# Kernel optimization log

Hardware: AMD Instinct MI355X
Metric: run time of the kernel (lower is better)

The kernel has to match this reference:

```python
import jax, jax.numpy as jnp
import numpy as np

N_NODES = 100000
N_EDGES = 1600000
IN_FEATS = 64
OUT_FEATS = 100


def setup_inputs() -> dict:
    key = jax.random.key(0)
    k1, k2, k3, k4 = jax.random.split(key, 4)
    e = jax.random.normal(k1, (N_EDGES, IN_FEATS), dtype=jnp.float32)
    dst = jax.random.randint(k2, (N_EDGES,), 0, N_NODES, dtype=jnp.int32)
    W = jax.random.normal(k3, (OUT_FEATS, IN_FEATS), dtype=jnp.float32) * (1.0 / np.sqrt(IN_FEATS))
    b = jax.random.normal(k4, (OUT_FEATS,), dtype=jnp.float32) * 0.01
    return {"e": e, "dst": dst, "W": W, "b": b, "n_nodes": N_NODES}


def reference(e, dst, W, b, n_nodes):
    # edge linear projection: f = e @ W^T + b  -> [n_edges, out_feats]
    f = jnp.einsum("ei,oi->eo", e, W) + b
    # copy_e + mean reduce: segment-mean of edge features into dst nodes
    sums = jax.ops.segment_sum(f, dst, num_segments=n_nodes)  # [n_nodes, out]
    deg = jax.ops.segment_sum(jnp.ones((f.shape[0],), dtype=f.dtype), dst,
                              num_segments=n_nodes)  # in-degree per node
    # DGL mean reducer yields 0 for zero-in-degree nodes
    h = sums / jnp.maximum(deg, 1.0)[:, None]
    return h
```

## Files before the change

### kernel.cpp

```cpp
#include <hip/hip_runtime.h>

#define N_NODES 100000
#define N_EDGES 1600000
#define IN_F    64
#define OUT_F   100

#define K_BUCKETS 1563
#define NBLK      500
#define EPB       3200
#define SCAN_LEN  (K_BUCKETS * NBLK)
#define SCH       2048
#define SB        ((SCAN_LEN + SCH - 1) / SCH)
#define CAP       3072

#define OFF_CNT   0
#define OFF_PART  (SCAN_LEN * 4)
#define OFF_BIN   (SCAN_LEN * 4 + 2048)
#define WS_NEEDED (OFF_BIN + N_EDGES * 4)

#define FB_DEG     0
#define FB_OFFS    524288
#define FB_CURSOR  1048576
#define FB_GCUR    1572864
#define FB_EIDS    1573888

__global__ void __launch_bounds__(256) k_count(const int* __restrict__ dst,
                                               int* __restrict__ cnt) {
    __shared__ int h[K_BUCKETS];
    for (int i = threadIdx.x; i < K_BUCKETS; i += 256) h[i] = 0;
    __syncthreads();
    int base = blockIdx.x * EPB;
    #pragma unroll
    for (int it = 0; it < 3; it++) {
        int i = base + it * 1024 + threadIdx.x * 4;
        int4 d = *(const int4*)(dst + i);
        atomicAdd(&h[d.x >> 6], 1);
        atomicAdd(&h[d.y >> 6], 1);
        atomicAdd(&h[d.z >> 6], 1);
        atomicAdd(&h[d.w >> 6], 1);
    }
    if (threadIdx.x < 128) {
        int i = base + 3072 + threadIdx.x;
        atomicAdd(&h[dst[i] >> 6], 1);
    }
    __syncthreads();
    for (int k = threadIdx.x; k < K_BUCKETS; k += 256)
        cnt[k * NBLK + blockIdx.x] = h[k];
}

__global__ void k_s1(const int* __restrict__ cnt, int* __restrict__ part) {
    __shared__ int ws_[4];
    int b0 = blockIdx.x * SCH;
    int t = threadIdx.x;
    int tot = 0;
    #pragma unroll
    for (int i = 0; i < 8; i++) {
        int idx = b0 + i * 256 + t;
        if (idx < SCAN_LEN) tot += cnt[idx];
    }
    #pragma unroll
    for (int off = 32; off; off >>= 1) tot += __shfl_down(tot, off, 64);
    if ((t & 63) == 0) ws_[t >> 6] = tot;
    __syncthreads();
    if (t == 0) part[blockIdx.x] = ws_[0] + ws_[1] + ws_[2] + ws_[3];
}

__global__ void k_s2(int* __restrict__ part) {
    int lane = threadIdx.x;
    int carry = 0;
    for (int b0 = 0; b0 < SB; b0 += 64) {
        int idx = b0 + lane;
        int v = (idx < SB) ? part[idx] : 0;
        int x = v;
        #pragma unroll
        for (int off = 1; off < 64; off <<= 1) {
            int y = __shfl_up(x, off, 64);
            if (lane >= off) x += y;
        }
        int tot = __shfl(x, 63, 64);
        if (idx < SB) part[idx] = carry + x - v;
        carry += tot;
    }
}

__global__ void k_s3(int* __restrict__ cnt, const int* __restrict__ part) {
    __shared__ int wsum[4];
    int t = threadIdx.x, lane = t & 63, w = t >> 6;
    int idx0 = blockIdx.x * SCH + t * 8;
    int v[8];
    int s = 0;
    #pragma unroll
    for (int i = 0; i < 8; i++) {
        v[i] = (idx0 + i < SCAN_LEN) ? cnt[idx0 + i] : 0;
        s += v[i];
    }
    int x = s;
    #pragma unroll
    for (int off = 1; off < 64; off <<= 1) {
        int y = __shfl_up(x, off, 64);
        if (lane >= off) x += y;
    }
    if (lane == 63) wsum[w] = x;
    __syncthreads();
    int wb = 0;
    for (int i = 0; i < w; i++) wb += wsum[i];
    int run = part[blockIdx.x] + wb + (x - s);
    #pragma unroll
    for (int i = 0; i < 8; i++) {
        int tmp = v[i];
        if (idx0 + i < SCAN_LEN) cnt[idx0 + i] = run;
        run += tmp;
    }
}

__global__ void __launch_bounds__(256) k_bin(const int* __restrict__ dst,
                                             const int* __restrict__ scn,
                                             int* __restrict__ binned) {
    __shared__ int cur[K_BUCKETS];
    for (int k = threadIdx.x; k < K_BUCKETS; k += 256)
        cur[k] = scn[k * NBLK + blockIdx.x];
    __syncthreads();
    int base = blockIdx.x * EPB;
    #pragma unroll
    for (int it = 0; it < 3; it++) {
        int i = base + it * 1024 + threadIdx.x * 4;
        int4 d = *(const int4*)(dst + i);
        int p;
        p = atomicAdd(&cur[d.x >> 6], 1); binned[p] = ((d.x & 63) << 21) | i;
        p = atomicAdd(&cur[d.y >> 6], 1); binned[p] = ((d.y & 63) << 21) | (i + 1);
        p = atomicAdd(&cur[d.z >> 6], 1); binned[p] = ((d.z & 63) << 21) | (i + 2);
        p = atomicAdd(&cur[d.w >> 6], 1); binned[p] = ((d.w & 63) << 21) | (i + 3);
    }
    if (threadIdx.x < 128) {
        int i = base + 3072 + threadIdx.x;
        int d = dst[i];
        int p = atomicAdd(&cur[d >> 6], 1);
        binned[p] = ((d & 63) << 21) | i;
    }
}

__global__ void __launch_bounds__(256, 2) k_fused(
        const float* __restrict__ e, const int* __restrict__ binned,
        const int* __restrict__ scn, const float* __restrict__ W,
        const float* __restrict__ b, float* __restrict__ out) {
    __shared__ int   deg[64];
    __shared__ int   lofs[64];
    __shared__ int   sorted[CAP];
    __shared__ __align__(16) float srow[4][64];

    int tid = threadIdx.x, lane = tid & 63, w = tid >> 6;
    int sub = lane & 15, g = lane >> 4;
    int bk = blockIdx.x;
    int base = scn[bk * NBLK];
    int end  = (bk + 1 < K_BUCKETS) ? scn[(bk + 1) * NBLK] : N_EDGES;
    int cntb = end - base;

    for (int i = tid; i < 64; i += 256) deg[i] = 0;
    __syncthreads();

    bool fast = (cntb <= CAP);
    if (fast) {
        int pk[12], rk[12];
        int nI = (cntb + 255) >> 8;
        for (int i = 0; i < nI; i++) {
            int idx = tid + i * 256;
            if (idx < cntb) {
                int p = binned[base + idx];
                pk[i] = p;
                rk[i] = atomicAdd(&deg[p >> 21], 1);
            } else pk[i] = -1;
        }
        __syncthreads();
        if (w == 0) {
            int d = deg[lane];
            int x = d;
            #pragma unroll
            for (int off = 1; off < 64; off <<= 1) {
                int y = __shfl_up(x, off, 64);
                if (lane >= off) x += y;
            }
            lofs[lane] = x - d;
        }
        __syncthreads();
        for (int i = 0; i < nI; i++) {
            if (pk[i] >= 0) {
                int lid = pk[i] >> 21;
                sorted[lofs[lid] + rk[i]] = pk[i] & 0x1FFFFF;
            }
        }
        __syncthreads();
    }

    int row1 = 64 + lane;
    if (row1 >= OUT_F) row1 = 0;
    float w0[IN_F], w1[IN_F];
    const float4* W4 = (const float4*)W;
    #pragma unroll
    for (int j = 0; j < IN_F / 4; j++) {
        float4 t0 = W4[lane * (IN_F / 4) + j];
        w0[4*j+0] = t0.x; w0[4*j+1] = t0.y; w0[4*j+2] = t0.z; w0[4*j+3] = t0.w;
        float4 t1 = W4[row1 * (IN_F / 4) + j];
        w1[4*j+0] = t1.x; w1[4*j+1] = t1.y; w1[4*j+2] = t1.z; w1[4*j+3] = t1.w;
    }
    float bb0 = b[lane];
    float bb1 = b[row1];

    const float4* e4 = (const float4*)e;

    for (int t = 0; t < 16; t++) {
        int lid = w * 16 + t;
        int node = bk * 64 + lid;
        if (node >= N_NODES) break;

        int c;
        float* sr = &srow[w][0];

        if (fast) {
            int o = lofs[lid];
            c = deg[lid];
            if (c > 0) {
                float4 a0 = {0,0,0,0}, a1 = {0,0,0,0}, a2 = {0,0,0,0}, a3 = {0,0,0,0};
                for (int cb = 0; cb < c; cb += 64) {
                    int cc = c - cb; if (cc > 64) cc = 64;
                    int ng = (cc + 3) >> 2;
                    int ob = o + cb;
                    for (int i = 0; i < ng; i += 4) {
                        int idx0 = (i + 0) * 4 + g;
                        int idx1 = (i + 1) * 4 + g;
                        int idx2 = (i + 2) * 4 + g;
                        int idx3 = (i + 3) * 4 + g;
                        int c1 = cc - 1;
                        int e0 = sorted[ob + ((idx0 < c1) ? idx0 : c1)];
                        int e1 = sorted[ob + ((idx1 < c1) ? idx1 : c1)];
                        int e2 = sorted[ob + ((idx2 < c1) ? idx2 : c1)];
                        int e3 = sorted[ob + ((idx3 < c1) ? idx3 : c1)];
                        float4 v0 = e4[(size_t)e0 * 16 + sub];
                        float4 v1 = e4[(size_t)e1 * 16 + sub];
                        float4 v2 = e4[(size_t)e2 * 16 + sub];
                        float4 v3 = e4[(size_t)e3 * 16 + sub];
                        float m0 = (idx0 < cc) ? 1.0f : 0.0f;
                        float m1 = (idx1 < cc) ? 1.0f : 0.0f;
                        float m2 = (idx2 < cc) ? 1.0f : 0.0f;
                        float m3 = (idx3 < cc) ? 1.0f : 0.0f;
                        a0.x = fmaf(v0.x, m0, a0.x); a0.y = fmaf(v0.y, m0, a0.y);
                        a0.z = fmaf(v0.z, m0, a0.z); a0.w = fmaf(v0.w, m0, a0.w);
                        a1.x = fmaf(v1.x, m1, a1.x); a1.y = fmaf(v1.y, m1, a1.y);
                        a1.z = fmaf(v1.z, m1, a1.z); a1.w = fmaf(v1.w, m1, a1.w);
                        a2.x = fmaf(v2.x, m2, a2.x); a2.y = fmaf(v2.y, m2, a2.y);
                        a2.z = fmaf(v2.z, m2, a2.z); a2.w = fmaf(v2.w, m2, a2.w);
                        a3.x = fmaf(v3.x, m3, a3.x); a3.y = fmaf(v3.y, m3, a3.y);
                        a3.z = fmaf(v3.z, m3, a3.z); a3.w = fmaf(v3.w, m3, a3.w);
                    }
                }
                float4 s;
                s.x = (a0.x + a1.x) + (a2.x + a3.x);
                s.y = (a0.y + a1.y) + (a2.y + a3.y);
                s.z = (a0.z + a1.z) + (a2.z + a3.z);
                s.w = (a0.w + a1.w) + (a2.w + a3.w);
                s.x += __shfl_xor(s.x, 16, 64);
                s.y += __shfl_xor(s.y, 16, 64);
                s.z += __shfl_xor(s.z, 16, 64);
                s.w += __shfl_xor(s.w, 16, 64);
                s.x += __shfl_xor(s.x, 32, 64);
                s.y += __shfl_xor(s.y, 32, 64);
                s.z += __shfl_xor(s.z, 32, 64);
                s.w += __shfl_xor(s.w, 32, 64);
                float inv = 1.0f / (float)c;
                s.x *= inv; s.y *= inv; s.z *= inv; s.w *= inv;
                if (g == 0) ((float4*)sr)[sub] = s;
            }
        } else {
            c = 0;
            float s0 = 0.f;
            for (int j0 = 0; j0 < cntb; j0 += 64) {
                int idx = j0 + lane;
                int p = (idx < cntb) ? binned[base + idx] : -1;
                bool m = (p >= 0) && ((p >> 21) == lid);
                unsigned long long msk = __ballot(m);
                c += __popcll(msk);
                while (msk) {
                    int l = __ffsll((long long)msk) - 1;
                    msk &= msk - 1;
                    int eid = __builtin_amdgcn_readlane(p, l) & 0x1FFFFF;
                    s0 += e[((size_t)eid << 6) + lane];
                }
            }
            if (c > 0) sr[lane] = s0 * (1.0f / (float)c);
        }

        float h0 = 0.0f, h1 = 0.0f;
        if (c > 0) {
            float aa0 = 0.f, aa1 = 0.f;
            const float4* sr4 = (const float4*)sr;
            #pragma unroll
            for (int q = 0; q < 16; q++) {
                float4 f = sr4[q];
                aa0 = fmaf(f.x, w0[4*q+0], aa0);  aa1 = fmaf(f.x, w1[4*q+0], aa1);
                aa0 = fmaf(f.y, w0[4*q+1], aa0);  aa1 = fmaf(f.y, w1[4*q+1], aa1);
                aa0 = fmaf(f.z, w0[4*q+2], aa0);  aa1 = fmaf(f.z, w1[4*q+2], aa1);
                aa0 = fmaf(f.w, w0[4*q+3], aa0);  aa1 = fmaf(f.w, w1[4*q+3], aa1);
            }
            h0 = aa0 + bb0;
            h1 = aa1 + bb1;
        }

        size_t ob2 = (size_t)node * OUT_F;
        out[ob2 + lane] = h0;
        if (lane < OUT_F - 64) out[ob2 + 64 + lane] = h1;
    }
}

__global__ void fb_hist(const int* __restrict__ dst, int* __restrict__ deg) {
    int i = (blockIdx.x * blockDim.x + threadIdx.x) * 4;
    if (i + 3 < N_EDGES) {
        int4 d = *(const int4*)(dst + i);
        atomicAdd(&deg[d.x], 1); atomicAdd(&deg[d.y], 1);
        atomicAdd(&deg[d.z], 1); atomicAdd(&deg[d.w], 1);
    } else {
        for (int k = i; k < N_EDGES; k++) atomicAdd(&deg[dst[k]], 1);
    }
}

__global__ void fb_scan(const int* __restrict__ deg, int* __restrict__ offs,
                        int* __restrict__ cursor, int* __restrict__ gcur) {
    int n = blockIdx.x * blockDim.x + threadIdx.x;
    int lane = threadIdx.x & 63;
    int d = (n < N_NODES) ? deg[n] : 0;
    int x = d;
    #pragma unroll
    for (int off = 1; off < 64; off <<= 1) {
        int y = __shfl_up(x, off, 64);
        if (lane >= off) x += y;
    }
    int excl = x - d;
    int total = __shfl(x, 63, 64);
    int bs = 0;
    if (lane == 63) bs = atomicAdd(gcur, total);
    bs = __shfl(bs, 63, 64);
    if (n < N_NODES) {
        offs[n] = bs + excl;
        cursor[n] = bs + excl;
    }
}

__global__ void fb_scatter(const int* __restrict__ dst, int* __restrict__ cursor,
                           int* __restrict__ eids) {
    int i = (blockIdx.x * blockDim.x + threadIdx.x) * 4;
    if (i + 3 < N_EDGES) {
        int4 d = *(const int4*)(dst + i);
        int p0 = atomicAdd(&cursor[d.x], 1);
        int p1 = atomicAdd(&cursor[d.y], 1);
        int p2 = atomicAdd(&cursor[d.z], 1);
        int p3 = atomicAdd(&cursor[d.w], 1);
        eids[p0] = i; eids[p1] = i + 1; eids[p2] = i + 2; eids[p3] = i + 3;
    } else {
        for (int k = i; k < N_EDGES; k++) {
            int pos = atomicAdd(&cursor[dst[k]], 1);
            eids[pos] = k;
        }
    }
}

__global__ void __launch_bounds__(256) fb_gather(
        const float* __restrict__ e, const int* __restrict__ eids,
        const int* __restrict__ offs, const int* __restrict__ deg,
        const float* __restrict__ W, const float* __restrict__ b,
        float* __restrict__ out, int n_waves_total) {
    __shared__ float srow[4][64];
    int lane = threadIdx.x & 63, w = (threadIdx.x >> 6) & 3;
    int wid  = (blockIdx.x * blockDim.x + threadIdx.x) >> 6;
    int row1 = 64 + lane;
    if (row1 >= OUT_F) row1 = 0;
    float w0[IN_F], w1[IN_F];
    const float4* W4 = (const float4*)W;
    #pragma unroll
    for (int j = 0; j < IN_F / 4; j++) {
        float4 t0 = W4[lane * (IN_F / 4) + j];
        w0[4*j+0] = t0.x; w0[4*j+1] = t0.y; w0[4*j+2] = t0.z; w0[4*j+3] = t0.w;
        float4 t1 = W4[row1 * (IN_F / 4) + j];
        w1[4*j+0] = t1.x; w1[4*j+1] = t1.y; w1[4*j+2] = t1.z; w1[4*j+3] = t1.w;
    }
    float bb0 = b[lane];
    float bb1 = b[row1];
    for (int n = wid; n < N_NODES; n += n_waves_total) {
        int o = __builtin_amdgcn_readfirstlane(offs[n]);
        int c = __builtin_amdgcn_readfirstlane(deg[n]);
        float s0 = 0.f, s1 = 0.f;
        for (int cb = 0; cb < c; cb += 64) {
            int cc = c - cb; if (cc > 64) cc = 64;
            int myeid = 0;
            if (lane < cc) myeid = eids[o + cb + lane];
            for (int j = 0; j < cc; j += 2) {
                int i0 = __builtin_amdgcn_readlane(myeid, j);
                s0 += e[((size_t)i0 << 6) + lane];
                if (j + 1 < cc) {
                    int i1 = __builtin_amdgcn_readlane(myeid, j + 1);
                    s1 += e[((size_t)i1 << 6) + lane];
                }
            }
        }
        float* sr = &srow[w][0];
        sr[lane] = (s0 + s1) * ((c > 0) ? 1.0f / (float)c : 0.0f);
        float a0 = 0.f, a1 = 0.f;
        const float4* sr4 = (const float4*)sr;
        #pragma unroll
        for (int q = 0; q < 16; q++) {
            float4 f = sr4[q];
            a0 = fmaf(f.x, w0[4*q+0], a0);  a1 = fmaf(f.x, w1[4*q+0], a1);
            a0 = fmaf(f.y, w0[4*q+1], a0);  a1 = fmaf(f.y, w1[4*q+1], a1);
            a0 = fmaf(f.z, w0[4*q+2], a0);  a1 = fmaf(f.z, w1[4*q+2], a1);
            a0 = fmaf(f.w, w0[4*q+3], a0);  a1 = fmaf(f.w, w1[4*q+3], a1);
        }
        float h0 = (c > 0) ? a0 + bb0 : 0.0f;
        float h1 = (c > 0) ? a1 + bb1 : 0.0f;
        size_t ob = (size_t)n * OUT_F;
        out[ob + lane] = h0;
        if (lane < OUT_F - 64) out[ob + 64 + lane] = h1;
    }
}

extern "C" void kernel_launch(void* const* d_in, const int* in_sizes, int n_in,
                              void* d_out, int out_size, void* d_ws, size_t ws_size,
                              hipStream_t stream) {
    const float* e   = (const float*)d_in[0];
    const int*   dst = (const int*)d_in[1];
    const float* W   = (const float*)d_in[2];
    const float* b   = (const float*)d_in[3];
    float* out = (float*)d_out;
    char* ws = (char*)d_ws;

    if (ws_size >= (size_t)WS_NEEDED) {
        int* cnt    = (int*)(ws + OFF_CNT);
        int* part   = (int*)(ws + OFF_PART);
        int* binned = (int*)(ws + OFF_BIN);

        k_count<<<NBLK, 256, 0, stream>>>(dst, cnt);
        k_s1   <<<SB, 256, 0, stream>>>(cnt, part);
        k_s2   <<<1, 64, 0, stream>>>(part);
        k_s3   <<<SB, 256, 0, stream>>>(cnt, part);
        k_bin  <<<NBLK, 256, 0, stream>>>(dst, cnt, binned);
        k_fused<<<K_BUCKETS, 256, 0, stream>>>(e, binned, cnt, W, b, out);
    } else {
        int* deg    = (int*)(ws + FB_DEG);
        int* offs   = (int*)(ws + FB_OFFS);
        int* cursor = (int*)(ws + FB_CURSOR);
        int* gcur   = (int*)(ws + FB_GCUR);
        int* eids   = (int*)(ws + FB_EIDS);

        hipMemsetAsync(deg, 0, N_NODES * sizeof(int), stream);
        hipMemsetAsync(gcur, 0, sizeof(int), stream);
        fb_hist   <<<(N_EDGES / 4 + 255) / 256, 256, 0, stream>>>(dst, deg);
        fb_scan   <<<(N_NODES + 255) / 256, 256, 0, stream>>>(deg, offs, cursor, gcur);
        fb_scatter<<<(N_EDGES / 4 + 255) / 256, 256, 0, stream>>>(dst, cursor, eids);
        fb_gather <<<8192, 256, 0, stream>>>(e, eids, offs, deg, W, b, out, 8192 * 4);
    }
}
```

Measured before the change: 648.2 us.

## Split fused gather-GEMV kernel into separate gather-mean and GEMV kernels

Splits the fused kernel in two. The first kernel gathers and averages the edge rows per node into a 64-wide workspace buffer and records each node's degree. The second kernel applies the 100x64 projection and bias to those averages. Taking the 128 weight registers out of the gather kernel lets it run at higher occupancy (launch bounds raised to 4) and better hide the latency of the irregular gather. The cost is an extra kernel launch and a write then read of the 100000x64 intermediate. The pk/rk loops are also fully unrolled so those arrays can stay in registers.

Measured after the change: 655.4 us. Within noise of the previous version (+1.1%).

```diff
diff --git a/kernel.cpp b/kernel.cpp
--- a/kernel.cpp
+++ b/kernel.cpp
@@ -16,7 +16,9 @@
 #define OFF_CNT   0
 #define OFF_PART  (SCAN_LEN * 4)
 #define OFF_BIN   (SCAN_LEN * 4 + 2048)
-#define WS_NEEDED (OFF_BIN + N_EDGES * 4)
+#define OFF_MSUM  (((OFF_BIN + N_EDGES * 4) + 255) & ~255)
+#define OFF_DEGO  (OFF_MSUM + N_NODES * IN_F * 4)
+#define WS_NEEDED ((size_t)OFF_DEGO + (size_t)N_NODES * 4)
 
 #define FB_DEG     0
 #define FB_OFFS    524288
@@ -139,14 +141,13 @@
     }
 }
 
-__global__ void __launch_bounds__(256, 2) k_fused(
+__global__ void __launch_bounds__(256, 4) k_gsum(
         const float* __restrict__ e, const int* __restrict__ binned,
-        const int* __restrict__ scn, const float* __restrict__ W,
-        const float* __restrict__ b, float* __restrict__ out) {
-    __shared__ int   deg[64];
-    __shared__ int   lofs[64];
-    __shared__ int   sorted[CAP];
-    __shared__ __align__(16) float srow[4][64];
+        const int* __restrict__ scn, float* __restrict__ msum,
+        int* __restrict__ degOut) {
+    __shared__ int deg[64];
+    __shared__ int lofs[64];
+    __shared__ int sorted[CAP];
 
     int tid = threadIdx.x, lane = tid & 63, w = tid >> 6;
     int sub = lane & 15, g = lane >> 4;
@@ -162,13 +163,17 @@
     if (fast) {
         int pk[12], rk[12];
         int nI = (cntb + 255) >> 8;
-        for (int i = 0; i < nI; i++) {
-            int idx = tid + i * 256;
-            if (idx < cntb) {
-                int p = binned[base + idx];
-                pk[i] = p;
-                rk[i] = atomicAdd(&deg[p >> 21], 1);
-            } else pk[i] = -1;
+        #pragma unroll
+        for (int i = 0; i < 12; i++) {
+            pk[i] = -1; rk[i] = 0;
+            if (i < nI) {
+                int idx = tid + i * 256;
+                if (idx < cntb) {
+                    int p = binned[base + idx];
+                    pk[i] = p;
+                    rk[i] = atomicAdd(&deg[p >> 21], 1);
+                }
+            }
         }
         __syncthreads();
         if (w == 0) {
@@ -182,42 +187,31 @@
             lofs[lane] = x - d;
         }
         __syncthreads();
-        for (int i = 0; i < nI; i++) {
+        #pragma unroll
+        for (int i = 0; i < 12; i++) {
             if (pk[i] >= 0) {
                 int lid = pk[i] >> 21;
                 sorted[lofs[lid] + rk[i]] = pk[i] & 0x1FFFFF;
             }
         }
         __syncthreads();
-    }
-
-    int row1 = 64 + lane;
-    if (row1 >= OUT_F) row1 = 0;
-    float w0[IN_F], w1[IN_F];
-    const float4* W4 = (const float4*)W;
-    #pragma unroll
-    for (int j = 0; j < IN_F / 4; j++) {
-        float4 t0 = W4[lane * (IN_F / 4) + j];
-        w0[4*j+0] = t0.x; w0[4*j+1] = t0.y; w0[4*j+2] = t0.z; w0[4*j+3] = t0.w;
-        float4 t1 = W4[row1 * (IN_F / 4) + j];
-        w1[4*j+0] = t1.x; w1[4*j+1] = t1.y; w1[4*j+2] = t1.z; w1[4*j+3] = t1.w;
-    }
-    float bb0 = b[lane];
-    float bb1 = b[row1];
+        if (w == 0) {
+            int node = bk * 64 + lane;
+            if (node < N_NODES) degOut[node] = deg[lane];
+        }
+    }
 
     const float4* e4 = (const float4*)e;
+    float4* msum4 = (float4*)msum;
 
     for (int t = 0; t < 16; t++) {
         int lid = w * 16 + t;
         int node = bk * 64 + lid;
         if (node >= N_NODES) break;
 
-        int c;
-        float* sr = &srow[w][0];
-
         if (fast) {
             int o = lofs[lid];
-            c = deg[lid];
+            int c = deg[lid];
             if (c > 0) {
                 float4 a0 = {0,0,0,0}, a1 = {0,0,0,0}, a2 = {0,0,0,0}, a3 = {0,0,0,0};
                 for (int cb = 0; cb < c; cb += 64) {
@@ -267,10 +261,10 @@
                 s.w += __shfl_xor(s.w, 32, 64);
                 float inv = 1.0f / (float)c;
                 s.x *= inv; s.y *= inv; s.z *= inv; s.w *= inv;
-                if (g == 0) ((float4*)sr)[sub] = s;
+                if (g == 0) msum4[(size_t)node * 16 + sub] = s;
             }
         } else {
-            c = 0;
+            int c = 0;
             float s0 = 0.f;
             for (int j0 = 0; j0 < cntb; j0 += 64) {
                 int idx = j0 + lane;
@@ -285,13 +279,56 @@
                     s0 += e[((size_t)eid << 6) + lane];
                 }
             }
-            if (c > 0) sr[lane] = s0 * (1.0f / (float)c);
-        }
-
+            if (c > 0) msum[(size_t)node * 64 + lane] = s0 * (1.0f / (float)c);
+            if (lane == 0) degOut[node] = c;
+        }
+    }
+}
+
+__global__ void __launch_bounds__(256, 2) k_gemv(
+        const float* __restrict__ msum, const int* __restrict__ degOut,
+        const float* __restrict__ W, const float* __restrict__ b,
+        float* __restrict__ out) {
+    __shared__ __align__(16) float srow[4][16 * 64];
+    int lane = threadIdx.x & 63, w = threadIdx.x >> 6;
+    int wave = blockIdx.x * 4 + w;
+    int base = wave * 16;
+    if (base >= N_NODES) return;
+    int nmax = N_NODES - base;
+    if (nmax > 16) nmax = 16;
+
+    int row1 = 64 + lane;
+    if (row1 >= OUT_F) row1 = 0;
+    float w0[IN_F], w1[IN_F];
+    const float4* W4 = (const float4*)W;
+    #pragma unroll
+    for (int j = 0; j < IN_F / 4; j++) {
+        float4 t0 = W4[lane * (IN_F / 4) + j];
+        w0[4*j+0] = t0.x; w0[4*j+1] = t0.y; w0[4*j+2] = t0.z; w0[4*j+3] = t0.w;
+        float4 t1 = W4[row1 * (IN_F / 4) + j];
+        w1[4*j+0] = t1.x; w1[4*j+1] = t1.y; w1[4*j+2] = t1.z; w1[4*j+3] = t1.w;
+    }
+    float bb0 = b[lane];
+    float bb1 = b[row1];
+
+    int d_l = 0;
+    if (lane < nmax) d_l = degOut[base + lane];
+
+    float4* s4 = (float4*)&srow[w][0];
+    const float4* m4 = (const float4*)msum + (size_t)base * 16;
+    int nf4 = nmax * 16;
+    #pragma unroll
+    for (int it = 0; it < 4; it++) {
+        int idx = it * 64 + lane;
+        if (idx < nf4) s4[idx] = m4[idx];
+    }
+
+    for (int j = 0; j < nmax; j++) {
+        int c = __shfl(d_l, j, 64);
         float h0 = 0.0f, h1 = 0.0f;
         if (c > 0) {
             float aa0 = 0.f, aa1 = 0.f;
-            const float4* sr4 = (const float4*)sr;
+            const float4* sr4 = (const float4*)&srow[w][j * 64];
             #pragma unroll
             for (int q = 0; q < 16; q++) {
                 float4 f = sr4[q];
@@ -303,7 +340,7 @@
             h0 = aa0 + bb0;
             h1 = aa1 + bb1;
         }
-
+        int node = base + j;
         size_t ob2 = (size_t)node * OUT_F;
         out[ob2 + lane] = h0;
         if (lane < OUT_F - 64) out[ob2 + 64 + lane] = h1;
@@ -429,17 +466,20 @@
     float* out = (float*)d_out;
     char* ws = (char*)d_ws;
 
-    if (ws_size >= (size_t)WS_NEEDED) {
-        int* cnt    = (int*)(ws + OFF_CNT);
-        int* part   = (int*)(ws + OFF_PART);
-        int* binned = (int*)(ws + OFF_BIN);
+    if (ws_size >= WS_NEEDED) {
+        int*   cnt    = (int*)(ws + OFF_CNT);
+        int*   part   = (int*)(ws + OFF_PART);
+        int*   binned = (int*)(ws + OFF_BIN);
+        float* msum   = (float*)(ws + OFF_MSUM);
+        int*   degOut = (int*)(ws + OFF_DEGO);
 
         k_count<<<NBLK, 256, 0, stream>>>(dst, cnt);
         k_s1   <<<SB, 256, 0, stream>>>(cnt, part);
         k_s2   <<<1, 64, 0, stream>>>(part);
         k_s3   <<<SB, 256, 0, stream>>>(cnt, part);
         k_bin  <<<NBLK, 256, 0, stream>>>(dst, cnt, binned);
-        k_fused<<<K_BUCKETS, 256, 0, stream>>>(e, binned, cnt, W, b, out);
+        k_gsum <<<K_BUCKETS, 256, 0, stream>>>(e, binned, cnt, msum, degOut);
+        k_gemv <<<(N_NODES / 16 + 3) / 4 + 1, 256, 0, stream>>>(msum, degOut, W, b, out);
     } else {
         int* deg    = (int*)(ws + FB_DEG);
         int* offs   = (int*)(ws + FB_OFFS);
```
